# Kernel optimization log

Measured on AMD Instinct MI355X. Metric: run time of the kernel, lower is better.

## Reference

```python
import jax, jax.numpy as jnp
import numpy as np

B, S, H, L = 64, 512, 768, 9


def setup_inputs() -> dict:
    key = jax.random.key(0)
    ks = jax.random.split(key, 8)
    hidden = jax.random.normal(ks[0], (B, S, H), jnp.float32)
    lengths = jax.random.randint(ks[1], (B,), S // 2, S + 1)
    attention_mask = (jnp.arange(S)[None, :] < lengths[:, None]).astype(jnp.int32)
    labels = jax.random.randint(ks[2], (B, S), 0, L)
    # sprinkle some -100 ignore labels like HF datasets do
    ignore = jax.random.uniform(ks[3], (B, S)) < 0.05
    labels = jnp.where(ignore, -100, labels)
    W = jax.random.normal(ks[4], (H, L), jnp.float32) * 0.02
    b = jnp.zeros((L,), jnp.float32)
    start_transitions = jax.random.uniform(ks[5], (L,), jnp.float32, -0.1, 0.1)
    end_transitions = jax.random.uniform(ks[6], (L,), jnp.float32, -0.1, 0.1)
    transitions = jax.random.uniform(ks[7], (L, L), jnp.float32, -0.1, 0.1)
    return dict(hidden=hidden, attention_mask=attention_mask, labels=labels, W=W, b=b,
                start_transitions=start_transitions, end_transitions=end_transitions,
                transitions=transitions)


def _crf_numerator(emissions, tags, maskf, start_t, end_t, trans):
    # score of the gold tag sequence (torchcrf _compute_score)
    first = start_t[tags[:, 0]] + jnp.take_along_axis(emissions[:, 0], tags[:, 0:1], axis=1)[:, 0]
    em = jnp.take_along_axis(emissions, tags[..., None], axis=2)[..., 0]      # [B,S]
    tr = trans[tags[:, :-1], tags[:, 1:]]                                     # [B,S-1]
    score = first + jnp.sum((em[:, 1:] + tr) * maskf[:, 1:], axis=1)
    last_idx = (jnp.sum(maskf, axis=1).astype(jnp.int32) - 1)
    last_tags = jnp.take_along_axis(tags, last_idx[:, None], axis=1)[:, 0]
    return score + end_t[last_tags]


def _crf_lognorm(emissions, maskf, start_t, end_t, trans):
    # forward algorithm (torchcrf _compute_normalizer) as a lax.scan
    score0 = start_t[None, :] + emissions[:, 0]                               # [B,L]
    em_seq = jnp.transpose(emissions[:, 1:], (1, 0, 2))                       # [S-1,B,L]
    m_seq = maskf[:, 1:].T                                                    # [S-1,B]

    def step(score, xs):
        em_t, m_t = xs
        nxt = jax.nn.logsumexp(score[:, :, None] + trans[None] + em_t[:, None, :], axis=1)
        return jnp.where(m_t[:, None] > 0, nxt, score), None

    score, _ = jax.lax.scan(step, score0, (em_seq, m_seq))
    return jax.nn.logsumexp(score + end_t[None, :], axis=1)


def _viterbi(emissions, maskf, start_t, end_t, trans):
    score0 = start_t[None, :] + emissions[:, 0]                               # [B,L]
    em_seq = jnp.transpose(emissions[:, 1:], (1, 0, 2))
    m_seq = maskf[:, 1:].T

    def step(score, xs):
        em_t, m_t = xs
        cand = score[:, :, None] + trans[None]                                # [B,L,L]
        bp = jnp.argmax(cand, axis=1)                                         # [B,L]
        nxt = jnp.max(cand, axis=1) + em_t
        return jnp.where(m_t[:, None] > 0, nxt, score), bp

    score, history = jax.lax.scan(step, score0, (em_seq, m_seq))              # history [S-1,B,L]
    best_last = jnp.argmax(score + end_t[None, :], axis=1)                    # [B]

    def back(cur, xs):
        bp_t, m_t = xs
        prev = jnp.where(m_t > 0, jnp.take_along_axis(bp_t, cur[:, None], axis=1)[:, 0], cur)
        return prev, prev

    _, tags_rev = jax.lax.scan(back, best_last, (history[::-1], m_seq[::-1]))
    tags = jnp.concatenate([tags_rev[::-1].T, best_last[:, None]], axis=1)    # [B,S]
    return tags


def reference(hidden, attention_mask, labels, W, b, start_transitions, end_transitions, transitions):
    maskf = attention_mask.astype(hidden.dtype)                               # [B,S]
    logits = jnp.einsum('bsh,hl->bsl', hidden, W) + b                         # [B,S,L]
    safe_labels = jnp.where(labels == -100, 0, labels)
    num = _crf_numerator(logits, safe_labels, maskf, start_transitions, end_transitions, transitions)
    den = _crf_lognorm(logits, maskf, start_transitions, end_transitions, transitions)
    loss = -jnp.mean(num - den)                                               # -crf(..., reduction='mean')
    tags = _viterbi(logits, maskf, start_transitions, end_transitions, transitions)
    fake_logits = jax.nn.one_hot(tags, L, dtype=logits.dtype) * maskf[..., None]
    return loss, fake_logits
```

## Files before the change

kernel.cpp:

```cpp
#include <hip/hip_runtime.h>
#include <hip/hip_bf16.h>
#include <stdint.h>

constexpr int BB  = 64;
constexpr int SS  = 512;
constexpr int HH  = 768;
constexpr int NL  = 9;
constexpr int NROWS = BB * SS;
constexpr int EMN   = SS * NL;
constexpr int NSEG  = 8;
constexpr float NEG  = -1e30f;

__device__ __forceinline__ float readlane_f(float v, int lane) {
  union { float f; int i; } u;
  u.f = v;
  u.i = __builtin_amdgcn_readlane(u.i, lane);
  return u.f;
}

__device__ __forceinline__ float max3f(float a, float b, float c) {
  float d;
  asm("v_max3_f32 %0, %1, %2, %3" : "=v"(d) : "v"(a), "v"(b), "v"(c));
  return d;
}

__device__ __forceinline__ float max9f(const float* c) {
  return max3f(max3f(c[0], c[1], c[2]),
               max3f(c[3], c[4], c[5]),
               max3f(c[6], c[7], c[8]));
}

__global__ __launch_bounds__(256, 2) void logits_kernel(
    const float* __restrict__ hidden, const float* __restrict__ W,
    const float* __restrict__ bias, const int* __restrict__ mask,
    float* __restrict__ logits, int* __restrict__ lens,
    float* __restrict__ out) {
  const int lane = threadIdx.x & 63;
  const int wid  = blockIdx.x * 4 + (threadIdx.x >> 6);

  if (blockIdx.x == 0 && threadIdx.x == 0) out[0] = 0.0f;

  if (blockIdx.x < 64 && threadIdx.x < 64) {
    const int4* mp = (const int4*)(mask + blockIdx.x * SS);
    const int4 a = mp[threadIdx.x];
    const int4 c = mp[threadIdx.x + 64];
    int lsum = a.x + a.y + a.z + a.w + c.x + c.y + c.z + c.w;
#pragma unroll
    for (int off = 32; off >= 1; off >>= 1) lsum += __shfl_xor(lsum, off, 64);
    if (threadIdx.x == 0) lens[blockIdx.x] = lsum;
  }

  float w[3][4][NL];
#pragma unroll
  for (int j = 0; j < 3; ++j)
#pragma unroll
    for (int k = 0; k < 4; ++k) {
      const int r = lane * 4 + j * 256 + k;
#pragma unroll
      for (int l = 0; l < NL; ++l) w[j][k][l] = W[r * NL + l];
    }
  const float my_bias = (lane < NL) ? bias[lane] : 0.0f;

  float4 h[4][3];
#pragma unroll
  for (int r = 0; r < 4; ++r) {
    const float4* hp = (const float4*)(hidden + (size_t)(wid + r * 8192) * HH);
#pragma unroll
    for (int j = 0; j < 3; ++j) h[r][j] = hp[lane + j * 64];
  }
  float acc[4][NL];
#pragma unroll
  for (int r = 0; r < 4; ++r)
#pragma unroll
    for (int l = 0; l < NL; ++l) acc[r][l] = 0.0f;
#pragma unroll
  for (int r = 0; r < 4; ++r)
#pragma unroll
    for (int j = 0; j < 3; ++j)
#pragma unroll
      for (int l = 0; l < NL; ++l)
        acc[r][l] += h[r][j].x * w[j][0][l] + h[r][j].y * w[j][1][l] +
                     h[r][j].z * w[j][2][l] + h[r][j].w * w[j][3][l];
#pragma unroll
  for (int off = 32; off >= 1; off >>= 1)
#pragma unroll
    for (int r = 0; r < 4; ++r)
#pragma unroll
      for (int l = 0; l < NL; ++l)
        acc[r][l] += __shfl_xor(acc[r][l], off, 64);
  if (lane < NL) {
#pragma unroll
    for (int r = 0; r < 4; ++r) {
      float v = acc[r][0];
#pragma unroll
      for (int l = 1; l < NL; ++l) if (lane == l) v = acc[r][l];
      logits[(size_t)(wid + r * 8192) * NL + lane] = v + my_bias;
    }
  }
}

__global__ __launch_bounds__(64) void scan_kernel(
    const float* __restrict__ logits, const int* __restrict__ labels,
    const float* __restrict__ start_t, const float* __restrict__ end_t,
    const float* __restrict__ trans, float* __restrict__ out,
    float* __restrict__ num_den, const int* __restrict__ lens,
    float* __restrict__ segmat) {
  __shared__ float4 embv[1161];
  __shared__ unsigned char bp_s[EMN + 80];
  __shared__ unsigned char tags_s[SS];
  __shared__ unsigned char lab[SS];

  const int blk = blockIdx.x;
  const int tid = threadIdx.x;
  const int j   = (tid < NL) ? tid : NL - 1;

  if (blk < 64) {
    __builtin_amdgcn_s_setprio(1);
    const int b   = blk;
    const int len = lens[b];
    const float* emb = logits + (size_t)b * EMN;

    {
      const float4* src = (const float4*)emb;
#pragma unroll
      for (int i = 0; i < 18; ++i) embv[tid + i * 64] = src[tid + i * 64];
    }
    __syncthreads();
    const float* emb_s = (const float*)embv;

    float tc[NL];
#pragma unroll
    for (int i = 0; i < NL; ++i) tc[i] = trans[i * NL + j];
    float s[NL];
#pragma unroll
    for (int i = 0; i < NL; ++i) s[i] = start_t[i] + emb_s[i];
    float eA = emb_s[1 * NL + j], eB = emb_s[2 * NL + j];
    float eC = emb_s[3 * NL + j], eD = emb_s[4 * NL + j];
    for (int t = 1; t < len; ++t) {
      float c[NL];
#pragma unroll
      for (int i = 0; i < NL; ++i) c[i] = s[i] + tc[i];
      const float best = max9f(c);
      const float nxt  = best + eA;
      {
        const bool b01 = c[0] >= c[1], b23 = c[2] >= c[3];
        const bool b45 = c[4] >= c[5], b67 = c[6] >= c[7];
        const float v01 = b01 ? c[0] : c[1]; const int i01 = b01 ? 0 : 1;
        const float v23 = b23 ? c[2] : c[3]; const int i23 = b23 ? 2 : 3;
        const float v45 = b45 ? c[4] : c[5]; const int i45 = b45 ? 4 : 5;
        const float v67 = b67 ? c[6] : c[7]; const int i67 = b67 ? 6 : 7;
        const bool bA = v01 >= v23, bB = v45 >= v67;
        const float vA = bA ? v01 : v23; const int iA = bA ? i01 : i23;
        const float vB = bB ? v45 : v67; const int iB = bB ? i45 : i67;
        const bool bC = vA >= vB;
        const float vC = bC ? vA : vB; const int iC = bC ? iA : iB;
        const bool bD = vC >= c[8];
        const int arg = bD ? iC : 8;
        bp_s[t * NL + tid] = (unsigned char)arg;
      }
#pragma unroll
      for (int i = 0; i < NL; ++i) s[i] = readlane_f(nxt, i);
      eA = eB; eB = eC; eC = eD;
      eD = emb_s[(t + 4) * NL + j];
    }
    float bv = s[0] + end_t[0];
    int   bl = 0;
#pragma unroll
    for (int i = 1; i < NL; ++i) {
      const float cc = s[i] + end_t[i];
      if (cc > bv) { bv = cc; bl = i; }
    }
    __syncthreads();

    uint64_t C = 0x876543210ULL;
#pragma unroll
    for (int k = 1; k <= 8; ++k) {
      const int t = 8 * tid + k;
      uint64_t nc = 0;
#pragma unroll
      for (int x = 0; x < 9; ++x) {
        const int g = bp_s[t * NL + x] & 15;
        nc |= ((C >> (4 * g)) & 15ULL) << (4 * x);
      }
      C = (t < len) ? nc : C;
    }
    const uint32_t Clo = (uint32_t)C, Chi = (uint32_t)(C >> 32);
    uint32_t cur = (uint32_t)bl;
    int bnd = 0;
#pragma unroll
    for (int c = 63; c >= 0; --c) {
      bnd = (tid == c) ? (int)cur : bnd;
      const uint32_t lo = (uint32_t)__builtin_amdgcn_readlane((int)Clo, c);
      const uint32_t hi = (uint32_t)__builtin_amdgcn_readlane((int)Chi, c);
      const uint64_t cc = ((uint64_t)hi << 32) | lo;
      cur = (uint32_t)((cc >> (4 * cur)) & 15u);
    }
    int tag = bnd;
#pragma unroll
    for (int k = 8; k >= 1; --k) {
      const int t = 8 * tid + k;
      const int tt = (t < 512) ? t : 511;
      const int nt = bp_s[tt * NL + tag];
      tag = (t < len) ? nt : tag;
      tags_s[t - 1] = (unsigned char)tag;
    }
    __syncthreads();
    for (int i = tid; i < EMN; i += 64) {
      const int t = i / NL;
      const int l = i - t * NL;
      out[1 + (size_t)b * EMN + i] =
          (t < len && l == (int)tags_s[t]) ? 1.0f : 0.0f;
    }

  } else if (blk < 128) {
    const int b   = blk - 64;
    const int len = lens[b];
    const float* emb = logits + (size_t)b * EMN;
    for (int t = tid; t < SS; t += 64) {
      const int v = labels[b * SS + t];
      lab[t] = (unsigned char)((v == -100) ? 0 : v);
    }
    __syncthreads();
    float contrib = 0.0f;
    for (int t = tid; t < SS; t += 64) {
      if (t >= 1 && t < len)
        contrib += emb[t * NL + lab[t]] + trans[lab[t - 1] * NL + lab[t]];
    }
#pragma unroll
    for (int off = 32; off >= 1; off >>= 1)
      contrib += __shfl_xor(contrib, off, 64);
    if (tid == 0) {
      const int l0 = lab[0];
      num_den[b] = start_t[l0] + emb[l0] + contrib + end_t[lab[len - 1]];
    }

  } else {
    const int id   = blk - 128;
    const int pair = id / 3;
    const int wv   = id - pair * 3;
    const int b    = pair >> 3;
    const int sg   = pair & 7;
    const int e0   = 3 * wv;
    const int len  = lens[b];
    const float* emb = logits + (size_t)b * EMN;
    float tc[NL];
#pragma unroll
    for (int i = 0; i < NL; ++i) tc[i] = trans[i * NL + j];
    float s0[NL], s1[NL], s2[NL];
#pragma unroll
    for (int i = 0; i < NL; ++i) {
      s0[i] = (i == e0)     ? 0.0f : NEG;
      s1[i] = (i == e0 + 1) ? 0.0f : NEG;
      s2[i] = (i == e0 + 2) ? 0.0f : NEG;
    }
    float my0 = (j == e0)     ? 0.0f : NEG;
    float my1 = (j == e0 + 1) ? 0.0f : NEG;
    float my2 = (j == e0 + 2) ? 0.0f : NEG;
    const int tbeg  = 64 * sg + 1;
    const int tlast = (64 * sg + 64 < 511) ? 64 * sg + 64 : 511;
    float eA = emb[tbeg * NL + j],       eB = emb[(tbeg + 1) * NL + j];
    float eC = emb[(tbeg + 2) * NL + j], eD = emb[(tbeg + 3) * NL + j];
    for (int t = tbeg; t <= tlast; ++t) {
      if (t >= len) break;
      float c0[NL], c1[NL], c2[NL];
#pragma unroll
      for (int i = 0; i < NL; ++i) {
        c0[i] = s0[i] + tc[i];
        c1[i] = s1[i] + tc[i];
        c2[i] = s2[i] + tc[i];
      }
      const float m0 = max9f(c0);
      const float m1 = max9f(c1);
      const float m2 = max9f(c2);
      float u0 = 0.0f, u1 = 0.0f, u2 = 0.0f;
#pragma unroll
      for (int i = 0; i < NL; ++i) {
        u0 += __expf(c0[i] - m0);
        u1 += __expf(c1[i] - m1);
        u2 += __expf(c2[i] - m2);
      }
      my0 = m0 + __logf(u0) + eA;
      my1 = m1 + __logf(u1) + eA;
      my2 = m2 + __logf(u2) + eA;
#pragma unroll
      for (int i = 0; i < NL; ++i) {
        s0[i] = readlane_f(my0, i);
        s1[i] = readlane_f(my1, i);
        s2[i] = readlane_f(my2, i);
      }
      eA = eB; eB = eC; eC = eD;
      eD = emb[(t + 4) * NL + j];
    }
    if (tid < NL) {
      float* M = segmat + (size_t)(b * NSEG + sg) * 81;
      M[(e0    ) * NL + tid] = my0;
      M[(e0 + 1) * NL + tid] = my1;
      M[(e0 + 2) * NL + tid] = my2;
    }
  }
}

__global__ __launch_bounds__(64) void combine_kernel(
    const float* __restrict__ logits, const float* __restrict__ segmat,
    const float* __restrict__ start_t, const float* __restrict__ end_t,
    const float* __restrict__ num_den, float* __restrict__ out) {
  const int b   = blockIdx.x;
  const int tid = threadIdx.x;
  const int j   = (tid < NL) ? tid : NL - 1;
  float s[NL];
#pragma unroll
  for (int i = 0; i < NL; ++i) s[i] = start_t[i] + logits[(size_t)b * EMN + i];
  float mcur[NL], mnxt[NL];
  {
    const float* M = segmat + (size_t)(b * NSEG) * 81;
#pragma unroll
    for (int i = 0; i < NL; ++i) mcur[i] = M[i * NL + j];
  }
  for (int sg = 0; sg < NSEG; ++sg) {
    if (sg + 1 < NSEG) {
      const float* M = segmat + (size_t)(b * NSEG + sg + 1) * 81;
#pragma unroll
      for (int i = 0; i < NL; ++i) mnxt[i] = M[i * NL + j];
    }
    float c[NL];
#pragma unroll
    for (int i = 0; i < NL; ++i) c[i] = s[i] + mcur[i];
    const float m = max9f(c);
    float sum = 0.0f;
#pragma unroll
    for (int i = 0; i < NL; ++i) sum += __expf(c[i] - m);
    const float nxt = m + __logf(sum);
#pragma unroll
    for (int i = 0; i < NL; ++i) s[i] = readlane_f(nxt, i);
#pragma unroll
    for (int i = 0; i < NL; ++i) mcur[i] = mnxt[i];
  }
  float c[NL];
#pragma unroll
  for (int i = 0; i < NL; ++i) c[i] = s[i] + end_t[i];
  const float m = max9f(c);
  float sum = 0.0f;
#pragma unroll
  for (int i = 0; i < NL; ++i) sum += __expf(c[i] - m);
  if (tid == 0) {
    const float den = m + __logf(sum);
    atomicAdd(out, (den - num_den[b]) * (1.0f / 64.0f));
  }
}

extern "C" void kernel_launch(void* const* d_in, const int* in_sizes, int n_in,
                              void* d_out, int out_size, void* d_ws, size_t ws_size,
                              hipStream_t stream) {
  const float* hidden  = (const float*)d_in[0];
  const int*   mask    = (const int*)d_in[1];
  const int*   labels  = (const int*)d_in[2];
  const float* W       = (const float*)d_in[3];
  const float* bias    = (const float*)d_in[4];
  const float* start_t = (const float*)d_in[5];
  const float* end_t   = (const float*)d_in[6];
  const float* trans   = (const float*)d_in[7];
  float* out = (float*)d_out;

  float* logits  = (float*)d_ws;
  float* segmat  = logits + (size_t)NROWS * NL;
  float* num_den = segmat + (size_t)BB * NSEG * 81;
  int*   lens    = (int*)(num_den + 128);

  logits_kernel<<<2048, 256, 0, stream>>>(hidden, W, bias, mask, logits, lens, out);
  scan_kernel<<<1664, 64, 0, stream>>>(logits, labels, start_t, end_t, trans,
                                       out, num_den, lens, segmat);
  combine_kernel<<<64, 64, 0, stream>>>(logits, segmat, start_t, end_t,
                                        num_den, out);
}
```

Baseline: 249.5 us.

## Stream Viterbi emissions from global into registers and pack backpointers as nibbles

The Viterbi block no longer stages the whole emission row into LDS before the recurrence. It now prefetches eight timesteps of emissions per lane from global memory into registers, double-buffered across 8-step chunks. Backpointers are packed four bits per step into 32-bit words, so each lane does one LDS store per chunk instead of a byte store every step, and the backtrace reads these packed words. This removes the upfront LDS copy and its barrier, and reduces LDS traffic on the serial critical path. In exchange, global-load latency must be hidden behind eight dependent steps, register pressure rises, and the per-step length check adds a branch inside the unrolled loop.

```diff
diff --git a/kernel.cpp b/kernel.cpp
--- a/kernel.cpp
+++ b/kernel.cpp
@@ -105,8 +105,7 @@
     const float* __restrict__ trans, float* __restrict__ out,
     float* __restrict__ num_den, const int* __restrict__ lens,
     float* __restrict__ segmat) {
-  __shared__ float4 embv[1161];
-  __shared__ unsigned char bp_s[EMN + 80];
+  __shared__ uint32_t bpw[64 * NL];
   __shared__ unsigned char tags_s[SS];
   __shared__ unsigned char lab[SS];
 
@@ -120,48 +119,57 @@
     const int len = lens[b];
     const float* emb = logits + (size_t)b * EMN;
 
-    {
-      const float4* src = (const float4*)emb;
-#pragma unroll
-      for (int i = 0; i < 18; ++i) embv[tid + i * 64] = src[tid + i * 64];
-    }
-    __syncthreads();
-    const float* emb_s = (const float*)embv;
-
     float tc[NL];
 #pragma unroll
     for (int i = 0; i < NL; ++i) tc[i] = trans[i * NL + j];
     float s[NL];
 #pragma unroll
-    for (int i = 0; i < NL; ++i) s[i] = start_t[i] + emb_s[i];
-    float eA = emb_s[1 * NL + j], eB = emb_s[2 * NL + j];
-    float eC = emb_s[3 * NL + j], eD = emb_s[4 * NL + j];
-    for (int t = 1; t < len; ++t) {
-      float c[NL];
-#pragma unroll
-      for (int i = 0; i < NL; ++i) c[i] = s[i] + tc[i];
-      const float best = max9f(c);
-      const float nxt  = best + eA;
-      {
-        const bool b01 = c[0] >= c[1], b23 = c[2] >= c[3];
-        const bool b45 = c[4] >= c[5], b67 = c[6] >= c[7];
-        const float v01 = b01 ? c[0] : c[1]; const int i01 = b01 ? 0 : 1;
-        const float v23 = b23 ? c[2] : c[3]; const int i23 = b23 ? 2 : 3;
-        const float v45 = b45 ? c[4] : c[5]; const int i45 = b45 ? 4 : 5;
-        const float v67 = b67 ? c[6] : c[7]; const int i67 = b67 ? 6 : 7;
-        const bool bA = v01 >= v23, bB = v45 >= v67;
-        const float vA = bA ? v01 : v23; const int iA = bA ? i01 : i23;
-        const float vB = bB ? v45 : v67; const int iB = bB ? i45 : i67;
-        const bool bC = vA >= vB;
-        const float vC = bC ? vA : vB; const int iC = bC ? iA : iB;
-        const bool bD = vC >= c[8];
-        const int arg = bD ? iC : 8;
-        bp_s[t * NL + tid] = (unsigned char)arg;
-      }
-#pragma unroll
-      for (int i = 0; i < NL; ++i) s[i] = readlane_f(nxt, i);
-      eA = eB; eB = eC; eC = eD;
-      eD = emb_s[(t + 4) * NL + j];
+    for (int i = 0; i < NL; ++i) s[i] = start_t[i] + emb[i];
+
+    float e0[8], e1[8];
+#pragma unroll
+    for (int k = 0; k < 8; ++k) e0[k] = emb[(1 + k) * NL + j];
+
+    for (int tb = 0; tb < 64; ++tb) {
+      const int tbase = 8 * tb;
+      if (tbase + 1 >= len) break;
+      if (tb < 63) {
+#pragma unroll
+        for (int k = 0; k < 8; ++k) e1[k] = emb[(tbase + 9 + k) * NL + j];
+      }
+      uint32_t wpk = 0;
+#pragma unroll
+      for (int k = 0; k < 8; ++k) {
+        const int t = tbase + 1 + k;
+        if (t < len) {
+          float c[NL];
+#pragma unroll
+          for (int i = 0; i < NL; ++i) c[i] = s[i] + tc[i];
+          const float best = max9f(c);
+          const float nxt  = best + e0[k];
+          {
+            const bool b01 = c[0] >= c[1], b23 = c[2] >= c[3];
+            const bool b45 = c[4] >= c[5], b67 = c[6] >= c[7];
+            const float v01 = b01 ? c[0] : c[1]; const int i01 = b01 ? 0 : 1;
+            const float v23 = b23 ? c[2] : c[3]; const int i23 = b23 ? 2 : 3;
+            const float v45 = b45 ? c[4] : c[5]; const int i45 = b45 ? 4 : 5;
+            const float v67 = b67 ? c[6] : c[7]; const int i67 = b67 ? 6 : 7;
+            const bool bA = v01 >= v23, bB = v45 >= v67;
+            const float vA = bA ? v01 : v23; const int iA = bA ? i01 : i23;
+            const float vB = bB ? v45 : v67; const int iB = bB ? i45 : i67;
+            const bool bC = vA >= vB;
+            const float vC = bC ? vA : vB; const int iC = bC ? iA : iB;
+            const bool bD = vC >= c[8];
+            const int arg = bD ? iC : 8;
+            wpk |= (uint32_t)arg << (4 * k);
+          }
+#pragma unroll
+          for (int i = 0; i < NL; ++i) s[i] = readlane_f(nxt, i);
+        }
+      }
+      if (tid < NL) bpw[tb * NL + tid] = wpk;
+#pragma unroll
+      for (int k = 0; k < 8; ++k) e0[k] = e1[k];
     }
     float bv = s[0] + end_t[0];
     int   bl = 0;
@@ -172,6 +180,9 @@
     }
     __syncthreads();
 
+    uint32_t wv_[NL];
+#pragma unroll
+    for (int x = 0; x < NL; ++x) wv_[x] = bpw[tid * NL + x];
     uint64_t C = 0x876543210ULL;
 #pragma unroll
     for (int k = 1; k <= 8; ++k) {
@@ -179,7 +190,7 @@
       uint64_t nc = 0;
 #pragma unroll
       for (int x = 0; x < 9; ++x) {
-        const int g = bp_s[t * NL + x] & 15;
+        const int g = (int)((wv_[x] >> (4 * (k - 1))) & 15u);
         nc |= ((C >> (4 * g)) & 15ULL) << (4 * x);
       }
       C = (t < len) ? nc : C;
@@ -200,7 +211,10 @@
     for (int k = 8; k >= 1; --k) {
       const int t = 8 * tid + k;
       const int tt = (t < 512) ? t : 511;
-      const int nt = bp_s[tt * NL + tag];
+      const int blk2 = (tt - 1) >> 3;
+      const int kk   = tt - 8 * blk2;
+      const uint32_t bw = bpw[blk2 * NL + tag];
+      const int nt = (int)((bw >> (4 * (kk - 1))) & 15u);
       tag = (t < len) ? nt : tag;
       tags_s[t - 1] = (unsigned char)tag;
     }
```

Result: faster. 240.9 us (-3.4%).
